# Kernel tuning notes

Hardware: AMD Instinct MI355X
Metric: run time of the kernel (lower is better)

Reference implementation:

```python
import jax, jax.numpy as jnp
import numpy as np

V, E, H, B, T = 50000, 300, 150, 64, 512  # vocab, embed_dim, hidden_dim, batch, seq_len
ATTN = H // 2


def setup_inputs() -> dict:
    key = jax.random.key(0)
    ks = jax.random.split(key, 18)
    s = 0.08
    inp = {
        "texts": jax.random.randint(ks[0], (B, T), 0, V, dtype=jnp.int32),
        "lengths": jax.random.randint(ks[1], (B,), 1, T + 1, dtype=jnp.int32),
        "emb_table": jax.random.normal(ks[2], (V, E), jnp.float32) * s,
        # layer 0 GRU (torch gate order: reset | update | new)
        "Wih0": jax.random.normal(ks[3], (3 * H, E), jnp.float32) * s,
        "Whh0": jax.random.normal(ks[4], (3 * H, H), jnp.float32) * s,
        "bih0": jax.random.normal(ks[5], (3 * H,), jnp.float32) * s,
        "bhh0": jax.random.normal(ks[6], (3 * H,), jnp.float32) * s,
        # layer 1 GRU
        "Wih1": jax.random.normal(ks[7], (3 * H, H), jnp.float32) * s,
        "Whh1": jax.random.normal(ks[8], (3 * H, H), jnp.float32) * s,
        "bih1": jax.random.normal(ks[9], (3 * H,), jnp.float32) * s,
        "bhh1": jax.random.normal(ks[10], (3 * H,), jnp.float32) * s,
        # additive attention
        "W1": jax.random.normal(ks[11], (ATTN, H), jnp.float32) * s,
        "w2": jax.random.normal(ks[12], (1, ATTN), jnp.float32) * s,
        # classifier head
        "fc1_w": jax.random.normal(ks[13], (H, H), jnp.float32) * s,
        "fc1_b": jax.random.normal(ks[14], (H,), jnp.float32) * s,
        "fc2_w": jax.random.normal(ks[15], (1, H), jnp.float32) * s,
        "fc2_b": jax.random.normal(ks[16], (1,), jnp.float32) * s,
    }
    return inp


def _gru_layer(x, Wih, Whh, bih, bhh, mask):
    # x: [T, B, I]; mask: [T, B, 1] True where t < length (packed-sequence semantics)
    h0 = jnp.zeros((x.shape[1], Whh.shape[1]), x.dtype)
    xw = x @ Wih.T + bih  # precompute input projections for all steps: [T, B, 3H]

    def step(h, inp):
        xw_t, m = inp
        hg = h @ Whh.T + bhh
        xr, xz, xn = jnp.split(xw_t, 3, axis=-1)
        hr, hz, hn = jnp.split(hg, 3, axis=-1)
        r = jax.nn.sigmoid(xr + hr)
        z = jax.nn.sigmoid(xz + hz)
        n = jnp.tanh(xn + r * hn)
        h_new = (1.0 - z) * n + z * h
        h_next = jnp.where(m, h_new, h)        # hidden freezes past length
        out = jnp.where(m, h_new, 0.0)          # pad_packed_sequence pads with zeros
        return h_next, out

    h_last, outs = jax.lax.scan(step, h0, (xw, mask))
    return outs, h_last


def reference(texts, lengths, emb_table, Wih0, Whh0, bih0, bhh0,
              Wih1, Whh1, bih1, bhh1, W1, w2, fc1_w, fc1_b, fc2_w, fc2_b):
    emb = emb_table[texts]                    # [B, T, E]
    x = jnp.transpose(emb, (1, 0, 2))         # [T, B, E] (batch_first=False)
    t_idx = jnp.arange(x.shape[0], dtype=lengths.dtype)
    mask = (t_idx[:, None] < lengths[None, :])[:, :, None]  # [T, B, 1]

    out0, _ = _gru_layer(x, Wih0, Whh0, bih0, bhh0, mask)
    out1, _ = _gru_layer(out0, Wih1, Whh1, bih1, bhh1, mask)  # [T, B, H]

    # additive attention over time (unmasked softmax, matching the original)
    scores = (jnp.tanh(out1 @ W1.T) @ w2.T)[..., 0].T        # [B, T]
    attn = jax.nn.softmax(scores, axis=1)                    # [B, T]
    ctx = jnp.einsum('bt,tbh->bh', attn, out1)               # [B, H]

    hcls = jax.nn.relu(ctx @ fc1_w.T + fc1_b)
    logits = (hcls @ fc2_w.T + fc2_b)[:, 0]                  # [B]
    return logits
```

## Files before the change

### kernel.cpp

```cpp
#include <hip/hip_runtime.h>

#define TT 512
#define BB 64
#define EE 300
#define HH 150
#define G3 450
#define AT 75
#define NW 28

typedef float v2f __attribute__((ext_vector_type(2)));

__device__ __forceinline__ float fast_rcp(float x) { return __builtin_amdgcn_rcpf(x); }
__device__ __forceinline__ float sigmoid_f(float x) { return fast_rcp(1.f + __expf(-x)); }
__device__ __forceinline__ float tanh_f(float x) {
  float e = __expf(2.f * x);
  return 1.f - 2.f * fast_rcp(e + 1.f);
}

__global__ void k_prep(const float* __restrict__ Wih0, const float* __restrict__ Whh0,
                       const float* __restrict__ Wih1, const float* __restrict__ Whh1,
                       const float* __restrict__ W1,   const float* __restrict__ fc1w,
                       float* __restrict__ Wih0T, float* __restrict__ Whh0T,
                       float* __restrict__ Wih1Tp, float* __restrict__ Whh1T,
                       float* __restrict__ W1T,   float* __restrict__ fc1T) {
  int tid = blockIdx.x * blockDim.x + threadIdx.x;
  int nt = gridDim.x * blockDim.x;
  for (int i = tid; i < G3 * EE; i += nt) { int r = i / EE, c = i - r * EE; Wih0T[c * G3 + r] = Wih0[i]; }
  for (int i = tid; i < G3 * HH; i += nt) { int r = i / HH, c = i - r * HH; Whh0T[c * G3 + r] = Whh0[i]; }
  for (int i = tid; i < 152 * G3; i += nt) {
    int k = i / G3, g = i - k * G3;
    Wih1Tp[i] = (k < HH) ? Wih1[g * HH + k] : 0.f;
  }
  for (int i = tid; i < G3 * HH; i += nt) { int r = i / HH, c = i - r * HH; Whh1T[c * G3 + r] = Whh1[i]; }
  for (int i = tid; i < AT * HH; i += nt) { int r = i / HH, c = i - r * HH; W1T[c * AT + r] = W1[i]; }
  for (int i = tid; i < HH * HH; i += nt) { int r = i / HH, c = i - r * HH; fc1T[c * HH + r] = fc1w[i]; }
}

__global__ __launch_bounds__(128, 2) void k_xw0(const int* __restrict__ texts,
                                                const int* __restrict__ lengths,
                                                const float* __restrict__ emb,
                                                const float* __restrict__ WihT,
                                                const float* __restrict__ bih,
                                                float* __restrict__ xw) {
  const int row0 = blockIdx.x * 32;
  if ((row0 & 511) >= lengths[row0 >> 9]) return;
  __shared__ __align__(16) float a_lds[32 * EE];
  const int tid = threadIdx.x;
  for (int p = tid; p < 32 * EE; p += 128) {
    int r = p / EE, e = p - r * EE;
    a_lds[p] = emb[(size_t)texts[row0 + r] * EE + e];
  }
  __syncthreads();
  const int g0 = tid, g1 = tid + 128, g2 = tid + 256;
  const bool has3 = (tid + 384) < G3;
  const int g3 = has3 ? tid + 384 : 0;
  float acc0[32], acc1[32], acc2[32], acc3[32];
#pragma unroll
  for (int r = 0; r < 32; ++r) { acc0[r] = 0.f; acc1[r] = 0.f; acc2[r] = 0.f; acc3[r] = 0.f; }
  const float4* a4 = reinterpret_cast<const float4*>(a_lds);
  for (int k = 0; k < EE; k += 4) {
    float wA[4], wB[4], wC[4], wD[4];
#pragma unroll
    for (int i = 0; i < 4; ++i) {
      const float* wr = WihT + (size_t)(k + i) * G3;
      wA[i] = wr[g0]; wB[i] = wr[g1]; wC[i] = wr[g2]; wD[i] = wr[g3];
    }
#pragma unroll
    for (int r = 0; r < 32; ++r) {
      const float4 av = a4[r * 75 + (k >> 2)];
      acc0[r] = fmaf(av.x, wA[0], acc0[r]); acc0[r] = fmaf(av.y, wA[1], acc0[r]);
      acc0[r] = fmaf(av.z, wA[2], acc0[r]); acc0[r] = fmaf(av.w, wA[3], acc0[r]);
      acc1[r] = fmaf(av.x, wB[0], acc1[r]); acc1[r] = fmaf(av.y, wB[1], acc1[r]);
      acc1[r] = fmaf(av.z, wB[2], acc1[r]); acc1[r] = fmaf(av.w, wB[3], acc1[r]);
      acc2[r] = fmaf(av.x, wC[0], acc2[r]); acc2[r] = fmaf(av.y, wC[1], acc2[r]);
      acc2[r] = fmaf(av.z, wC[2], acc2[r]); acc2[r] = fmaf(av.w, wC[3], acc2[r]);
      acc3[r] = fmaf(av.x, wD[0], acc3[r]); acc3[r] = fmaf(av.y, wD[1], acc3[r]);
      acc3[r] = fmaf(av.z, wD[2], acc3[r]); acc3[r] = fmaf(av.w, wD[3], acc3[r]);
    }
  }
  const float b0 = bih[g0], b1 = bih[g1], b2 = bih[g2], b3 = bih[g3];
#pragma unroll
  for (int r = 0; r < 32; ++r) {
    float* o = xw + (size_t)(row0 + r) * G3;
    o[g0] = acc0[r] + b0; o[g1] = acc1[r] + b1; o[g2] = acc2[r] + b2;
    if (has3) o[g3] = acc3[r] + b3;
  }
}

__global__ __launch_bounds__(128, 2) void k_xw1(const float* __restrict__ in,
                                                const int* __restrict__ lengths,
                                                const float* __restrict__ WihTp,
                                                const float* __restrict__ bih,
                                                float* __restrict__ xw) {
  const int row0 = blockIdx.x * 32;
  if ((row0 & 511) >= lengths[row0 >> 9]) return;
  __shared__ __align__(16) float a_lds[32 * 152];
  const int tid = threadIdx.x;
  for (int p = tid; p < 32 * 152; p += 128) {
    int r = p / 152, e = p - r * 152;
    a_lds[p] = (e < HH) ? in[(size_t)(row0 + r) * HH + e] : 0.f;
  }
  __syncthreads();
  const int g0 = tid, g1 = tid + 128, g2 = tid + 256;
  const bool has3 = (tid + 384) < G3;
  const int g3 = has3 ? tid + 384 : 0;
  float acc0[32], acc1[32], acc2[32], acc3[32];
#pragma unroll
  for (int r = 0; r < 32; ++r) { acc0[r] = 0.f; acc1[r] = 0.f; acc2[r] = 0.f; acc3[r] = 0.f; }
  const float4* a4 = reinterpret_cast<const float4*>(a_lds);
  for (int k = 0; k < 152; k += 4) {
    float wA[4], wB[4], wC[4], wD[4];
#pragma unroll
    for (int i = 0; i < 4; ++i) {
      const float* wr = WihTp + (size_t)(k + i) * G3;
      wA[i] = wr[g0]; wB[i] = wr[g1]; wC[i] = wr[g2]; wD[i] = wr[g3];
    }
#pragma unroll
    for (int r = 0; r < 32; ++r) {
      const float4 av = a4[r * 38 + (k >> 2)];
      acc0[r] = fmaf(av.x, wA[0], acc0[r]); acc0[r] = fmaf(av.y, wA[1], acc0[r]);
      acc0[r] = fmaf(av.z, wA[2], acc0[r]); acc0[r] = fmaf(av.w, wA[3], acc0[r]);
      acc1[r] = fmaf(av.x, wB[0], acc1[r]); acc1[r] = fmaf(av.y, wB[1], acc1[r]);
      acc1[r] = fmaf(av.z, wB[2], acc1[r]); acc1[r] = fmaf(av.w, wB[3], acc1[r]);
      acc2[r] = fmaf(av.x, wC[0], acc2[r]); acc2[r] = fmaf(av.y, wC[1], acc2[r]);
      acc2[r] = fmaf(av.z, wC[2], acc2[r]); acc2[r] = fmaf(av.w, wC[3], acc2[r]);
      acc3[r] = fmaf(av.x, wD[0], acc3[r]); acc3[r] = fmaf(av.y, wD[1], acc3[r]);
      acc3[r] = fmaf(av.z, wD[2], acc3[r]); acc3[r] = fmaf(av.w, wD[3], acc3[r]);
    }
  }
  const float b0 = bih[g0], b1 = bih[g1], b2 = bih[g2], b3 = bih[g3];
#pragma unroll
  for (int r = 0; r < 32; ++r) {
    float* o = xw + (size_t)(row0 + r) * G3;
    o[g0] = acc0[r] + b0; o[g1] = acc1[r] + b1; o[g2] = acc2[r] + b2;
    if (has3) o[g3] = acc3[r] + b3;
  }
}

__global__ __launch_bounds__(512, 2) void k_rec(const float* __restrict__ WhhT,
                                                const float* __restrict__ bhh,
                                                const float* __restrict__ xw,
                                                const int* __restrict__ lengths,
                                                float* __restrict__ out) {
  const int b = blockIdx.x;
  const int tid = threadIdx.x;
  __shared__ __align__(16) float h_lds[152];
  __shared__ float part[2][G3 + 6];
  const int len = lengths[b];

  int g = tid / 150;
  const bool worker = g < 3;
  const int gg = worker ? g : 2;
  const int j = worker ? (tid - 150 * g) : 0;
  const int kreal_end = (gg == 2) ? 150 : 48 * (gg + 1);
  const int h4base = 12 * gg;

  v2f w[3][NW];
#pragma unroll
  for (int r = 0; r < 3; ++r) {
    const int row = j + 150 * r;
#pragma unroll
    for (int q = 0; q < NW; ++q) {
      const int k0 = 48 * gg + 2 * q;
      const int k1 = k0 + 1;
      w[r][q][0] = (worker && k0 < kreal_end) ? WhhT[k0 * G3 + row] : 0.f;
      w[r][q][1] = (worker && k1 < kreal_end) ? WhhT[k1 * G3 + row] : 0.f;
    }
  }
  const float bias_r = bhh[j];
  const float bias_z = bhh[j + 150];
  const float bias_n = bhh[j + 300];

  for (int p = tid; p < 152; p += 512) h_lds[p] = 0.f;
  float h_reg = 0.f;
  __syncthreads();

  const float* xwb = xw + (size_t)b * TT * G3;
  float* outb = out + (size_t)b * TT * HH;
  const float4* h4 = reinterpret_cast<const float4*>(h_lds);

  for (int t = 0; t < len; ++t) {
    float xr = 0.f, xz = 0.f, xn = 0.f;
    if (tid < HH) {
      const float* xwt = xwb + (size_t)t * G3;
      xr = xwt[tid]; xz = xwt[tid + HH]; xn = xwt[tid + 2 * HH];
    }
    v2f ar0 = {0.f, 0.f}, ar1 = {0.f, 0.f};
    v2f az0 = {0.f, 0.f}, az1 = {0.f, 0.f};
    v2f an0 = {0.f, 0.f}, an1 = {0.f, 0.f};
#pragma unroll
    for (int q = 0; q < 14; ++q) {
      const float4 hv = h4[h4base + q];
      const v2f hx = {hv.x, hv.y};
      const v2f hy = {hv.z, hv.w};
      ar0 = __builtin_elementwise_fma(w[0][2 * q],     hx, ar0);
      ar1 = __builtin_elementwise_fma(w[0][2 * q + 1], hy, ar1);
      az0 = __builtin_elementwise_fma(w[1][2 * q],     hx, az0);
      az1 = __builtin_elementwise_fma(w[1][2 * q + 1], hy, az1);
      an0 = __builtin_elementwise_fma(w[2][2 * q],     hx, an0);
      an1 = __builtin_elementwise_fma(w[2][2 * q + 1], hy, an1);
    }
    const float pr = (ar0[0] + ar0[1]) + (ar1[0] + ar1[1]);
    const float pz = (az0[0] + az0[1]) + (az1[0] + az1[1]);
    const float pn = (an0[0] + an0[1]) + (an1[0] + an1[1]);
    if (worker && g > 0) {
      part[g - 1][j] = pr;
      part[g - 1][j + 150] = pz;
      part[g - 1][j + 300] = pn;
    }
    __syncthreads();

    if (tid < HH) {
      const float hr = pr + part[0][tid] + part[1][tid] + bias_r;
      const float hz = pz + part[0][tid + 150] + part[1][tid + 150] + bias_z;
      const float hn = pn + part[0][tid + 300] + part[1][tid + 300] + bias_n;
      const float r = sigmoid_f(xr + hr);
      const float z = sigmoid_f(xz + hz);
      const float n = tanh_f(xn + r * hn);
      const float hnew = (1.f - z) * n + z * h_reg;
      h_reg = hnew;
      h_lds[tid] = hnew;
      outb[(size_t)t * HH + tid] = hnew;
    }
    __syncthreads();
  }
  const int rem = (TT - len) * HH;
  float* outp = outb + (size_t)len * HH;
  for (int p = tid; p < rem; p += 512) outp[p] = 0.f;
}

__global__ __launch_bounds__(256) void k_scores(const float* __restrict__ out1,
                                                const int* __restrict__ lengths,
                                                const float* __restrict__ W1T,
                                                const float* __restrict__ w2,
                                                float* __restrict__ scores) {
  const int row0 = blockIdx.x * 32;
  const int tid = threadIdx.x;
  if ((row0 & 511) >= lengths[row0 >> 9]) {
    if (tid < 32) scores[row0 + tid] = 0.f;
    return;
  }
  __shared__ float sc[32];
  if (tid < 32) sc[tid] = 0.f;
  __syncthreads();
  for (int p = tid; p < 32 * AT; p += 256) {
    const int r = p / AT, a = p - r * AT;
    const float* x = out1 + (size_t)(row0 + r) * HH;
    float a0 = 0.f, a1 = 0.f;
    for (int k = 0; k < HH; k += 2) {
      a0 = fmaf(W1T[k * AT + a], x[k], a0);
      a1 = fmaf(W1T[(k + 1) * AT + a], x[k + 1], a1);
    }
    atomicAdd(&sc[r], tanh_f(a0 + a1) * w2[a]);
  }
  __syncthreads();
  if (tid < 32) scores[row0 + tid] = sc[tid];
}

__global__ __launch_bounds__(512) void k_final(const float* __restrict__ out1,
                                               const float* __restrict__ scores,
                                               const float* __restrict__ fc1T,
                                               const float* __restrict__ fc1b,
                                               const float* __restrict__ fc2w,
                                               const float* __restrict__ fc2b,
                                               float* __restrict__ logits) {
  const int b = blockIdx.x;
  const int tid = threadIdx.x;
  __shared__ float attn[TT];
  __shared__ float red[16];
  __shared__ float ctx[152];
  __shared__ float h1[152];

  float sv = scores[b * TT + tid];
  float m = sv;
#pragma unroll
  for (int off = 32; off > 0; off >>= 1) m = fmaxf(m, __shfl_xor(m, off));
  const int wave = tid >> 6;
  if ((tid & 63) == 0) red[wave] = m;
  __syncthreads();
  if (tid == 0) {
    float mm = red[0];
#pragma unroll
    for (int i = 1; i < 8; ++i) mm = fmaxf(mm, red[i]);
    red[8] = mm;
  }
  __syncthreads();
  const float e = __expf(sv - red[8]);
  attn[tid] = e;
  float zz = e;
#pragma unroll
  for (int off = 32; off > 0; off >>= 1) zz += __shfl_xor(zz, off);
  if ((tid & 63) == 0) red[wave] = zz;
  __syncthreads();
  if (tid == 0) {
    float ss = 0.f;
#pragma unroll
    for (int i = 0; i < 8; ++i) ss += red[i];
    red[9] = ss;
  }
  __syncthreads();
  const float invZ = 1.f / red[9];

  if (tid < HH) {
    const float* o1b = out1 + (size_t)b * TT * HH;
    float c0 = 0.f, c1 = 0.f, c2 = 0.f, c3 = 0.f;
    for (int t = 0; t < TT; t += 4) {
      c0 = fmaf(attn[t + 0], o1b[(t + 0) * HH + tid], c0);
      c1 = fmaf(attn[t + 1], o1b[(t + 1) * HH + tid], c1);
      c2 = fmaf(attn[t + 2], o1b[(t + 2) * HH + tid], c2);
      c3 = fmaf(attn[t + 3], o1b[(t + 3) * HH + tid], c3);
    }
    ctx[tid] = ((c0 + c1) + (c2 + c3)) * invZ;
  }
  __syncthreads();
  if (tid < HH) {
    float d0 = 0.f, d1 = 0.f;
    for (int k = 0; k < HH; k += 2) {
      d0 = fmaf(fc1T[k * HH + tid], ctx[k], d0);
      d1 = fmaf(fc1T[(k + 1) * HH + tid], ctx[k + 1], d1);
    }
    h1[tid] = fmaxf(d0 + d1 + fc1b[tid], 0.f);
  }
  __syncthreads();
  if (tid == 0) {
    float acc = fc2b[0];
    for (int k = 0; k < HH; ++k) acc = fmaf(fc2w[k], h1[k], acc);
    logits[b] = acc;
  }
}

extern "C" void kernel_launch(void* const* d_in, const int* in_sizes, int n_in,
                              void* d_out, int out_size, void* d_ws, size_t ws_size,
                              hipStream_t stream) {
  const int* texts     = (const int*)d_in[0];
  const int* lengths   = (const int*)d_in[1];
  const float* emb     = (const float*)d_in[2];
  const float* Wih0    = (const float*)d_in[3];
  const float* Whh0    = (const float*)d_in[4];
  const float* bih0    = (const float*)d_in[5];
  const float* bhh0    = (const float*)d_in[6];
  const float* Wih1    = (const float*)d_in[7];
  const float* Whh1    = (const float*)d_in[8];
  const float* bih1    = (const float*)d_in[9];
  const float* bhh1    = (const float*)d_in[10];
  const float* W1      = (const float*)d_in[11];
  const float* w2      = (const float*)d_in[12];
  const float* fc1w    = (const float*)d_in[13];
  const float* fc1b    = (const float*)d_in[14];
  const float* fc2w    = (const float*)d_in[15];
  const float* fc2b    = (const float*)d_in[16];
  float* logits = (float*)d_out;

  float* ws = (float*)d_ws;
  size_t off = 0;
  auto alloc = [&](size_t n) { float* p = ws + off; off += (n + 3) & ~(size_t)3; return p; };
  float* Wih0T  = alloc((size_t)G3 * EE);
  float* Whh0T  = alloc((size_t)G3 * HH);
  float* Wih1Tp = alloc((size_t)G3 * 152);
  float* Whh1T  = alloc((size_t)G3 * HH);
  float* W1T    = alloc((size_t)AT * HH);
  float* fc1T   = alloc((size_t)HH * HH);
  float* xwbuf  = alloc((size_t)BB * TT * G3);
  float* out0   = alloc((size_t)BB * TT * HH);
  float* out1   = alloc((size_t)BB * TT * HH);
  float* scores = alloc((size_t)BB * TT);
  (void)ws_size; (void)in_sizes; (void)n_in; (void)out_size;

  hipLaunchKernelGGL(k_prep, dim3(256), dim3(256), 0, stream,
                     Wih0, Whh0, Wih1, Whh1, W1, fc1w,
                     Wih0T, Whh0T, Wih1Tp, Whh1T, W1T, fc1T);
  hipLaunchKernelGGL(k_xw0, dim3((BB * TT) / 32), dim3(128), 0, stream, texts, lengths, emb, Wih0T, bih0, xwbuf);
  hipLaunchKernelGGL(k_rec, dim3(BB), dim3(512), 0, stream, Whh0T, bhh0, xwbuf, lengths, out0);
  hipLaunchKernelGGL(k_xw1, dim3((BB * TT) / 32), dim3(128), 0, stream, out0, lengths, Wih1Tp, bih1, xwbuf);
  hipLaunchKernelGGL(k_rec, dim3(BB), dim3(512), 0, stream, Whh1T, bhh1, xwbuf, lengths, out1);
  hipLaunchKernelGGL(k_scores, dim3((BB * TT) / 32), dim3(256), 0, stream, out1, lengths, W1T, w2, scores);
  hipLaunchKernelGGL(k_final, dim3(BB), dim3(512), 0, stream, out1, scores, fc1T, fc1b, fc2w, fc2b, logits);
}
```

Before: 1.145 ms.

## Tile attention score kernel with LDS-staged rows and register accumulators

Rewrites the attention score kernel so each 32-row tile of GRU output is staged in shared memory, and each of 75 threads computes one attention unit across all 32 rows using register accumulators and float4 reads. The shared-memory atomic reduction is replaced by a per-row partial buffer summed afterwards. This cuts redundant global reads of the weight matrix and row data and removes atomics. In exchange only 75 of 128 threads do the math, and the 32-wide accumulator array raises register pressure.

```diff
diff --git a/kernel.cpp b/kernel.cpp
--- a/kernel.cpp
+++ b/kernel.cpp
@@ -229,32 +229,67 @@
   for (int p = tid; p < rem; p += 512) outp[p] = 0.f;
 }
 
-__global__ __launch_bounds__(256) void k_scores(const float* __restrict__ out1,
-                                                const int* __restrict__ lengths,
-                                                const float* __restrict__ W1T,
-                                                const float* __restrict__ w2,
-                                                float* __restrict__ scores) {
+__global__ __launch_bounds__(128, 2) void k_scores(const float* __restrict__ out1,
+                                                   const int* __restrict__ lengths,
+                                                   const float* __restrict__ W1T,
+                                                   const float* __restrict__ w2,
+                                                   float* __restrict__ scores) {
   const int row0 = blockIdx.x * 32;
   const int tid = threadIdx.x;
   if ((row0 & 511) >= lengths[row0 >> 9]) {
     if (tid < 32) scores[row0 + tid] = 0.f;
     return;
   }
-  __shared__ float sc[32];
-  if (tid < 32) sc[tid] = 0.f;
-  __syncthreads();
-  for (int p = tid; p < 32 * AT; p += 256) {
-    const int r = p / AT, a = p - r * AT;
-    const float* x = out1 + (size_t)(row0 + r) * HH;
-    float a0 = 0.f, a1 = 0.f;
-    for (int k = 0; k < HH; k += 2) {
-      a0 = fmaf(W1T[k * AT + a], x[k], a0);
-      a1 = fmaf(W1T[(k + 1) * AT + a], x[k + 1], a1);
-    }
-    atomicAdd(&sc[r], tanh_f(a0 + a1) * w2[a]);
-  }
-  __syncthreads();
-  if (tid < 32) scores[row0 + tid] = sc[tid];
+  __shared__ __align__(16) float a_lds[32 * 152];
+  __shared__ float pp[32][77];
+  for (int p = tid; p < 32 * 152; p += 128) {
+    int r = p / 152, e = p - r * 152;
+    a_lds[p] = (e < HH) ? out1[(size_t)(row0 + r) * HH + e] : 0.f;
+  }
+  __syncthreads();
+  if (tid < AT) {
+    const int a = tid;
+    float acc[32];
+#pragma unroll
+    for (int r = 0; r < 32; ++r) acc[r] = 0.f;
+    const float4* a4 = reinterpret_cast<const float4*>(a_lds);
+    for (int k = 0; k < 148; k += 4) {
+      const float w0 = W1T[(k + 0) * AT + a];
+      const float w1 = W1T[(k + 1) * AT + a];
+      const float w2v = W1T[(k + 2) * AT + a];
+      const float w3 = W1T[(k + 3) * AT + a];
+#pragma unroll
+      for (int r = 0; r < 32; ++r) {
+        const float4 av = a4[r * 38 + (k >> 2)];
+        acc[r] = fmaf(av.x, w0, acc[r]);
+        acc[r] = fmaf(av.y, w1, acc[r]);
+        acc[r] = fmaf(av.z, w2v, acc[r]);
+        acc[r] = fmaf(av.w, w3, acc[r]);
+      }
+    }
+    {
+      const float w0 = W1T[148 * AT + a];
+      const float w1 = W1T[149 * AT + a];
+#pragma unroll
+      for (int r = 0; r < 32; ++r) {
+        acc[r] = fmaf(a_lds[r * 152 + 148], w0, acc[r]);
+        acc[r] = fmaf(a_lds[r * 152 + 149], w1, acc[r]);
+      }
+    }
+    const float wa = w2[a];
+#pragma unroll
+    for (int r = 0; r < 32; ++r) pp[r][a] = tanh_f(acc[r]) * wa;
+  }
+  __syncthreads();
+  if (tid < 32) {
+    float s0 = 0.f, s1 = 0.f, s2 = 0.f;
+    for (int a = 0; a < 75; a += 3) {
+      s0 += pp[tid][a];
+      s1 += pp[tid][a + 1];
+      s2 += pp[tid][a + 2];
+    }
+    scores[row0 + tid] = (s0 + s1) + s2;
+  }
 }
 
 __global__ __launch_bounds__(512) void k_final(const float* __restrict__ out1,
@@ -373,6 +408,6 @@
   hipLaunchKernelGGL(k_rec, dim3(BB), dim3(512), 0, stream, Whh0T, bhh0, xwbuf, lengths, out0);
   hipLaunchKernelGGL(k_xw1, dim3((BB * TT) / 32), dim3(128), 0, stream, out0, lengths, Wih1Tp, bih1, xwbuf);
   hipLaunchKernelGGL(k_rec, dim3(BB), dim3(512), 0, stream, Whh1T, bhh1, xwbuf, lengths, out1);
-  hipLaunchKernelGGL(k_scores, dim3((BB * TT) / 32), dim3(256), 0, stream, out1, lengths, W1T, w2, scores);
+  hipLaunchKernelGGL(k_scores, dim3((BB * TT) / 32), dim3(128), 0, stream, out1, lengths, W1T, w2, scores);
   hipLaunchKernelGGL(k_final, dim3(BB), dim3(512), 0, stream, out1, scores, fc1T, fc1b, fc2w, fc2b, logits);
 }
```

New measurement: 1.069 ms. 1.07x faster.
